# Optimization experiments

Measured on AMD Instinct MI355X. Metric: run time of the kernel, lower is better.

## Reference

```python
import jax, jax.numpy as jnp
import numpy as np

B, N, H, W = 8, 16384, 64, 64
CTX, OUT, ST = 32, 2, 1
HID = [516, 256, 128, 64, 32, 16]
IN_SIZE = CTX + 2 + ST + OUT  # 37


def _bilinear_sample(img, coord):
    """torch F.grid_sample, mode=bilinear, padding=zeros, align_corners=False.
    img: [B,C,H,W]; coord: [B,N,2] (x,y in [-1,1]). Returns [B,C,N]."""
    _, _, Hh, Ww = img.shape
    gx = (coord[..., 0] + 1.0) * (Ww * 0.5) - 0.5
    gy = (coord[..., 1] + 1.0) * (Hh * 0.5) - 0.5
    x0 = jnp.floor(gx)
    y0 = jnp.floor(gy)
    wx1 = gx - x0
    wy1 = gy - y0

    def tap(xi, yi, w):
        valid = (xi >= 0) & (xi < Ww) & (yi >= 0) & (yi < Hh)
        xc = jnp.clip(xi, 0, Ww - 1).astype(jnp.int32)
        yc = jnp.clip(yi, 0, Hh - 1).astype(jnp.int32)
        vals = jax.vmap(lambda im, y, x: im[:, y, x])(img, yc, xc)  # [B,C,N]
        return vals * (w * valid)[:, None, :]

    return (tap(x0, y0, (1 - wx1) * (1 - wy1))
            + tap(x0 + 1, y0, wx1 * (1 - wy1))
            + tap(x0, y0 + 1, (1 - wx1) * wy1)
            + tap(x0 + 1, y0 + 1, wx1 * wy1))


def _layer_shapes():
    shapes = [(IN_SIZE, HID[0])]
    for i in range(len(HID) - 1):
        shapes.append((HID[i] + IN_SIZE, HID[i + 1]))
    shapes.append((HID[-1], OUT))
    return shapes


def setup_inputs():
    key = jax.random.key(0)
    ks = jax.random.split(key, 4 + 7)
    inp = {
        "lr_fields": jax.random.normal(ks[0], (B, OUT, H, W), jnp.float32),
        "context_grid": jax.random.normal(ks[1], (B, CTX, H, W), jnp.float32),
        "hr_eps": jax.random.normal(ks[2], (B, H, W), jnp.float32),
        "coord": jax.random.uniform(ks[3], (B, N, 2), jnp.float32, -1.0, 1.0),
    }
    for j, (fi, fo) in enumerate(_layer_shapes()):
        inp[f"W{j}"] = jax.random.normal(ks[4 + j], (fi, fo), jnp.float32) / np.sqrt(fi)
        inp[f"b{j}"] = jnp.zeros((fo,), jnp.float32)
    return inp


def reference(lr_fields, context_grid, hr_eps, coord,
              W0, b0, W1, b1, W2, b2, W3, b3, W4, b4, W5, b5, W6, b6):
    # original permutes (0,1,3,2) before grid_sample -> swap spatial axes
    ctx_pts = _bilinear_sample(jnp.swapaxes(context_grid, 2, 3), coord)  # [B,CTX,N]
    lr_pts = _bilinear_sample(jnp.swapaxes(lr_fields, 2, 3), coord)      # [B,OUT,N]
    eps_pts = _bilinear_sample(jnp.swapaxes(hr_eps[:, None], 2, 3), coord)  # [B,1,N]
    x_in = jnp.concatenate([
        jnp.transpose(ctx_pts, (0, 2, 1)),
        coord,
        jnp.transpose(lr_pts, (0, 2, 1)),
        jnp.transpose(eps_pts, (0, 2, 1)),
    ], axis=2)  # [B,N,37]
    x = jax.nn.relu(x_in @ W0 + b0)
    for Wl, bl in ((W1, b1), (W2, b2), (W3, b3), (W4, b4), (W5, b5)):
        x = jax.nn.relu(jnp.concatenate([x, x_in], axis=2) @ Wl + bl)
    return x @ W6 + b6  # [B,N,2]
```

## Files before the change

kernel.cpp:

```cpp
#include <hip/hip_runtime.h>


#define NTH     1024
#define NWAVES  16
#define MPTS    64
#define MTILES  (MPTS / 16)
#define SROW    616
#define XIN_OFF 0
#define HSEG    64
#define NPOINTS (8 * 16384)
#define GRIDX   (NPOINTS / MPTS)
#define LDSBYTES (MPTS * SROW * 2)
#define CLSTRIDE 40
#define CLOFF   524288

typedef short          short8  __attribute__((ext_vector_type(8)));
typedef short          short4v __attribute__((ext_vector_type(4)));
typedef float          f32x4   __attribute__((ext_vector_type(4)));
typedef unsigned short u16;

__device__ __forceinline__ u16 f2bf(float f) {
    unsigned int u = __builtin_bit_cast(unsigned int, f);
    u += 0x7fffu + ((u >> 16) & 1u);
    return (u16)(u >> 16);
}

__device__ __forceinline__ unsigned cvtpk(float a, float b) {
    unsigned r;
    asm("v_cvt_pk_bf16_f32 %0, %1, %2" : "=v"(r) : "v"(a), "v"(b));
    return r;
}

__constant__ int pk_base8[8] = {0, 4224, 23680, 28800, 30336, 30848, 31040, 31104};
__constant__ int pk_ks[7]    = {2, 19, 10, 6, 4, 3, 1};
__constant__ int pk_khp[7]   = {0, 544, 256, 128, 64, 32, 32};
__constant__ int pk_kact[7]  = {0, 516, 256, 128, 64, 32, 16};
__constant__ int pk_nact[7]  = {516, 256, 128, 64, 32, 16, 2};

struct WPtrs { const float* W[7]; };

__global__ void pack_weights(WPtrs wp, u16* __restrict__ out)
{
    const int f = blockIdx.x * blockDim.x + threadIdx.x;
    if (f >= 31104) return;
    int l = 0;
    while (l < 6 && f >= pk_base8[l + 1]) ++l;
    const int r    = f - pk_base8[l];
    const int lane = r & 63;
    const int t    = r >> 6;
    const int ks   = pk_ks[l];
    const int s    = t % ks;
    const int nt   = t / ks;
    const int n    = nt * 16 + (lane & 15);
    const int k0   = s * 32 + (lane >> 4) * 8;
    const int nact = pk_nact[l];
    const int khp  = pk_khp[l];
    const int kact = pk_kact[l];
    const float* W = wp.W[l];

    union { short8 v; u16 e[8]; } frag;
#pragma unroll
    for (int j = 0; j < 8; ++j) {
        const int k = k0 + j;
        float v = 0.0f;
        if (n < nact) {
            if (k < khp) {
                if (k < kact) v = W[k * nact + n];
            } else {
                const int xr = k - khp;
                if (xr < 37) v = W[(kact + xr) * nact + n];
            }
        }
        frag.e[j] = f2bf(v);
    }
    *(short8*)(out + (size_t)f * 8) = frag.v;
}

struct RPk { const float* ctx; const float* lr; const float* eps; float* cl; };

__global__ void repack_cl(RPk q)
{
    __shared__ float ls[64 * CLSTRIDE];
    const int b = blockIdx.x >> 6;
    const int x = blockIdx.x & 63;
    for (int i = threadIdx.x; i < 64 * CLSTRIDE; i += 256) ls[i] = 0.f;
    __syncthreads();
    for (int i = threadIdx.x; i < 35 * 64; i += 256) {
        const int c = i / 64, y = i % 64;
        float v; int slot;
        if (c < 32)      { v = q.ctx[(((size_t)b * 32 + c) * 64 + x) * 64 + y]; slot = c; }
        else if (c < 34) { v = q.lr [(((size_t)b * 2 + (c - 32)) * 64 + x) * 64 + y]; slot = 34 + (c - 32); }
        else             { v = q.eps[(((size_t)b) * 64 + x) * 64 + y];          slot = 36; }
        ls[y * CLSTRIDE + slot] = v;
    }
    __syncthreads();
    float* out = q.cl + ((size_t)b * 64 + x) * 64 * CLSTRIDE;
    for (int i = threadIdx.x; i < 64 * CLSTRIDE; i += 256) out[i] = ls[i];
}

struct MainParams {
    const float* lr;
    const float* ctx;
    const float* eps;
    const float* coord;
    const float* Bb[7];
    const u16*   wpack;
    const float* cl;
    int          clok;
    float*       out;
};

template<int NACT, bool RELU>
__device__ __forceinline__ void store_nt(const f32x4* accm,
                                         const float* __restrict__ bias,
                                         u16* __restrict__ s_act,
                                         int nt, int mbase, int lm, int lq)
{
    const int bn = nt * 16 + lq * 4;
    float bv[4];
    if (bn + 4 <= NACT) {
        const f32x4 b4 = *(const f32x4*)(bias + bn);
        bv[0] = b4[0]; bv[1] = b4[1]; bv[2] = b4[2]; bv[3] = b4[3];
    } else {
#pragma unroll
        for (int r = 0; r < 4; ++r)
            bv[r] = (bn + r < NACT) ? bias[bn + r] : 0.f;
    }
#pragma unroll
    for (int m = 0; m < 2; ++m) {
        float v[4];
#pragma unroll
        for (int r = 0; r < 4; ++r) {
            v[r] = accm[m][r] + bv[r];
            if (RELU) v[r] = fmaxf(v[r], 0.f);
        }
        uint2 o;
        o.x = cvtpk(v[0], v[1]);
        o.y = cvtpk(v[2], v[3]);
        *(uint2*)(s_act + (size_t)((mbase + m) * 16 + lm) * SROW + HSEG + bn) = o;
    }
}

template<int KHP, int NT, int NACT, int LBASE,
         bool XIN, bool RELU, bool GOUT, bool IPBAR>
__device__ __forceinline__ void mlayer(const u16* __restrict__ wpack,
                                       const float* __restrict__ bias,
                                       u16* __restrict__ s_act,
                                       float* __restrict__ gout, int p0,
                                       int wave, int lane)
{
    constexpr int KHS = KHP / 32;
    constexpr int KS  = KHS + (XIN ? 2 : 0);
    const int lm = lane & 15;
    const int lq = lane >> 4;
    const int mg = wave & 1;
    const int ng = wave >> 1;
    const int mbase = mg * 2;

    const u16* arow0 = s_act + (size_t)((mbase * 16) + lm) * SROW + lq * 8;
    const u16* arow1 = arow0 + (size_t)16 * SROW;
    const u16* wl = wpack + LBASE + lane * 8;

#define ABOFF(s_) (((s_) < KHS) ? (HSEG + (s_) * 32) : (XIN_OFF + ((s_) - KHS) * 32))

    if constexpr (IPBAR) {
        const int nt0 = ng, nt1 = ng + 8;
        const bool act0 = nt0 < NT;
        const bool act1 = nt1 < NT;
        f32x4 acc[2][2];
#pragma unroll
        for (int i = 0; i < 2; ++i)
#pragma unroll
            for (int m = 0; m < 2; ++m)
                acc[i][m] = (f32x4){0.f, 0.f, 0.f, 0.f};

        if (act0) {
            const u16* bp0 = wl + (size_t)nt0 * KS * 512;
            const u16* bp1 = wl + (size_t)nt1 * KS * 512;
#pragma unroll
            for (int s = 0; s < KS; ++s) {
                const int ab = ABOFF(s);
                const short8 a0 = *(const short8*)(arow0 + ab);
                const short8 a1 = *(const short8*)(arow1 + ab);
                const short8 w0 = *(const short8*)(bp0 + (size_t)s * 512);
                acc[0][0] = __builtin_amdgcn_mfma_f32_16x16x32_bf16(w0, a0, acc[0][0], 0, 0, 0);
                acc[0][1] = __builtin_amdgcn_mfma_f32_16x16x32_bf16(w0, a1, acc[0][1], 0, 0, 0);
                if (act1) {
                    const short8 w1 = *(const short8*)(bp1 + (size_t)s * 512);
                    acc[1][0] = __builtin_amdgcn_mfma_f32_16x16x32_bf16(w1, a0, acc[1][0], 0, 0, 0);
                    acc[1][1] = __builtin_amdgcn_mfma_f32_16x16x32_bf16(w1, a1, acc[1][1], 0, 0, 0);
                }
            }
        }
        __syncthreads();
        if (act0) store_nt<NACT, RELU>(acc[0], bias, s_act, nt0, mbase, lm, lq);
        if (act1) store_nt<NACT, RELU>(acc[1], bias, s_act, nt1, mbase, lm, lq);
    } else {
        for (int g = 0;; ++g) {
            const int nt0 = ng + 16 * g;
            if (nt0 >= NT) break;
            const int nt1 = nt0 + 8;
            const bool act1 = nt1 < NT;
            f32x4 acc[2][2];
#pragma unroll
            for (int i = 0; i < 2; ++i)
#pragma unroll
                for (int m = 0; m < 2; ++m)
                    acc[i][m] = (f32x4){0.f, 0.f, 0.f, 0.f};

            const u16* bp0 = wl + (size_t)nt0 * KS * 512;
            const u16* bp1 = wl + (size_t)nt1 * KS * 512;
#pragma unroll
            for (int s = 0; s < KS; ++s) {
                const int ab = ABOFF(s);
                const short8 a0 = *(const short8*)(arow0 + ab);
                const short8 a1 = *(const short8*)(arow1 + ab);
                const short8 w0 = *(const short8*)(bp0 + (size_t)s * 512);
                acc[0][0] = __builtin_amdgcn_mfma_f32_16x16x32_bf16(w0, a0, acc[0][0], 0, 0, 0);
                acc[0][1] = __builtin_amdgcn_mfma_f32_16x16x32_bf16(w0, a1, acc[0][1], 0, 0, 0);
                if (act1) {
                    const short8 w1 = *(const short8*)(bp1 + (size_t)s * 512);
                    acc[1][0] = __builtin_amdgcn_mfma_f32_16x16x32_bf16(w1, a0, acc[1][0], 0, 0, 0);
                    acc[1][1] = __builtin_amdgcn_mfma_f32_16x16x32_bf16(w1, a1, acc[1][1], 0, 0, 0);
                }
            }

            if (GOUT) {
                if (lq == 0) {
                    const float b0 = bias[0], b1 = bias[1];
#pragma unroll
                    for (int m = 0; m < 2; ++m) {
                        float2 o;
                        o.x = acc[0][m][0] + b0;
                        o.y = acc[0][m][1] + b1;
                        *(float2*)(gout + (size_t)(p0 + (mbase + m) * 16 + lm) * 2) = o;
                    }
                }
            } else {
                store_nt<NACT, RELU>(acc[0], bias, s_act, nt0, mbase, lm, lq);
                if (act1)
                    store_nt<NACT, RELU>(acc[1], bias, s_act, nt1, mbase, lm, lq);
            }
        }
    }
#undef ABOFF
}

__global__ __launch_bounds__(NTH, 8)
void cont_decoder_mfma(MainParams p)
{
    extern __shared__ u16 s_act[];
    __shared__ int   s_x0[MPTS], s_y0[MPTS];
    __shared__ float s_wx[MPTS], s_wy[MPTS];

    const int tid  = threadIdx.x;
    const int wave = tid >> 6;
    const int lane = tid & 63;
    const int p0   = blockIdx.x * MPTS;
    const int b    = p0 >> 14;

    for (int i = tid; i < MPTS * 43; i += NTH) {
        const int pt = i / 43, c = i % 43;
        const int col = (c < 27) ? (37 + c) : (592 + (c - 27));
        s_act[pt * SROW + col] = 0;
    }

    if (tid < MPTS) {
        const int pt = p0 + tid;
        const float cx = p.coord[2 * pt];
        const float cy = p.coord[2 * pt + 1];
        const float gx = (cx + 1.0f) * 32.0f - 0.5f;
        const float gy = (cy + 1.0f) * 32.0f - 0.5f;
        const float fx0 = floorf(gx), fy0 = floorf(gy);
        s_x0[tid] = (int)fx0;
        s_y0[tid] = (int)fy0;
        s_wx[tid] = gx - fx0;
        s_wy[tid] = gy - fy0;
        s_act[tid * SROW + 32] = f2bf(cx);
        s_act[tid * SROW + 33] = f2bf(cy);
    }
    __syncthreads();

    if (p.clok) {
        const float* cl = p.cl + (size_t)b * 64 * 64 * CLSTRIDE;
        for (int idx = tid; idx < MPTS * 10; idx += NTH) {
            const int t = idx / 10;
            const int q = idx % 10;

            const int   x0 = s_x0[t], y0 = s_y0[t];
            const float wx = s_wx[t], wy = s_wy[t];
            const int x1 = x0 + 1, y1 = y0 + 1;
            const bool xv0 = (x0 >= 0) & (x0 < 64);
            const bool xv1 = (x1 >= 0) & (x1 < 64);
            const bool yv0 = (y0 >= 0) & (y0 < 64);
            const bool yv1 = (y1 >= 0) & (y1 < 64);
            const int xc0 = min(max(x0, 0), 63), xc1 = min(max(x1, 0), 63);
            const int yc0 = min(max(y0, 0), 63), yc1 = min(max(y1, 0), 63);

            const float w00 = (1.0f - wx) * (1.0f - wy) * ((xv0 && yv0) ? 1.0f : 0.0f);
            const float w10 = wx * (1.0f - wy)          * ((xv1 && yv0) ? 1.0f : 0.0f);
            const float w01 = (1.0f - wx) * wy          * ((xv0 && yv1) ? 1.0f : 0.0f);
            const float w11 = wx * wy                   * ((xv1 && yv1) ? 1.0f : 0.0f);

            const int qo = q * 4;
            const f32x4 t00 = *(const f32x4*)(cl + (size_t)(xc0 * 64 + yc0) * CLSTRIDE + qo);
            const f32x4 t10 = *(const f32x4*)(cl + (size_t)(xc1 * 64 + yc0) * CLSTRIDE + qo);
            const f32x4 t01 = *(const f32x4*)(cl + (size_t)(xc0 * 64 + yc1) * CLSTRIDE + qo);
            const f32x4 t11 = *(const f32x4*)(cl + (size_t)(xc1 * 64 + yc1) * CLSTRIDE + qo);

            const f32x4 v = w00 * t00 + w10 * t10 + w01 * t01 + w11 * t11;
            const unsigned lo = cvtpk(v[0], v[1]);
            const unsigned hi = cvtpk(v[2], v[3]);

            if (q == 8) {
                *(unsigned*)(s_act + (size_t)t * SROW + 34) = hi;
            } else {
                uint2 o; o.x = lo; o.y = hi;
                *(uint2*)(s_act + (size_t)t * SROW + qo) = o;
            }
        }
    } else {
        for (int idx = tid; idx < MPTS * 35; idx += NTH) {
            const int t = idx / 35;
            const int c = idx % 35;
            const float* base;
            int col;
            if (c < 32)      { base = p.ctx + (size_t)(b * 32 + c) * 4096;       col = c; }
            else if (c < 34) { base = p.lr  + (size_t)(b * 2 + (c - 32)) * 4096; col = 34 + (c - 32); }
            else             { base = p.eps + (size_t)b * 4096;                   col = 36; }

            const int   x0 = s_x0[t], y0 = s_y0[t];
            const float wx = s_wx[t], wy = s_wy[t];
            const int x1 = x0 + 1, y1 = y0 + 1;
            const bool xv0 = (x0 >= 0) & (x0 < 64);
            const bool xv1 = (x1 >= 0) & (x1 < 64);
            const bool yv0 = (y0 >= 0) & (y0 < 64);
            const bool yv1 = (y1 >= 0) & (y1 < 64);
            const int xc0 = min(max(x0, 0), 63), xc1 = min(max(x1, 0), 63);
            const int yc0 = min(max(y0, 0), 63), yc1 = min(max(y1, 0), 63);

            const float w00 = (1.0f - wx) * (1.0f - wy) * ((xv0 && yv0) ? 1.0f : 0.0f);
            const float w10 = wx * (1.0f - wy)          * ((xv1 && yv0) ? 1.0f : 0.0f);
            const float w01 = (1.0f - wx) * wy          * ((xv0 && yv1) ? 1.0f : 0.0f);
            const float w11 = wx * wy                   * ((xv1 && yv1) ? 1.0f : 0.0f);

            const float val = w00 * base[xc0 * 64 + yc0]
                            + w10 * base[xc1 * 64 + yc0]
                            + w01 * base[xc0 * 64 + yc1]
                            + w11 * base[xc1 * 64 + yc1];
            s_act[t * SROW + col] = f2bf(val);
        }
    }
    __syncthreads();

    mlayer<  0, 33, 516, 0,      true,  true,  false, false>(p.wpack, p.Bb[0], s_act, nullptr, p0, wave, lane);
    __syncthreads();
    mlayer<544, 16, 256, 33792,  true,  true,  false, true >(p.wpack, p.Bb[1], s_act, nullptr, p0, wave, lane);
    __syncthreads();
    mlayer<256,  8, 128, 189440, true,  true,  false, true >(p.wpack, p.Bb[2], s_act, nullptr, p0, wave, lane);
    __syncthreads();
    mlayer<128,  4,  64, 230400, true,  true,  false, true >(p.wpack, p.Bb[3], s_act, nullptr, p0, wave, lane);
    __syncthreads();
    mlayer< 64,  2,  32, 242688, true,  true,  false, true >(p.wpack, p.Bb[4], s_act, nullptr, p0, wave, lane);
    __syncthreads();
    mlayer< 32,  1,  16, 246784, true,  true,  false, true >(p.wpack, p.Bb[5], s_act, nullptr, p0, wave, lane);
    __syncthreads();
    mlayer< 32,  1,   2, 248320, false, false, true,  false>(p.wpack, p.Bb[6], s_act, p.out,   p0, wave, lane);
}

extern "C" void kernel_launch(void* const* d_in, const int* in_sizes, int n_in,
                              void* d_out, int out_size, void* d_ws, size_t ws_size,
                              hipStream_t stream)
{
    WPtrs wp;
    for (int l = 0; l < 7; ++l) wp.W[l] = (const float*)d_in[4 + 2 * l];

    const size_t cl_bytes = (size_t)8 * 64 * 64 * CLSTRIDE * 4;
    const bool clok = ws_size >= (size_t)CLOFF + cl_bytes;

    MainParams p;
    p.lr    = (const float*)d_in[0];
    p.ctx   = (const float*)d_in[1];
    p.eps   = (const float*)d_in[2];
    p.coord = (const float*)d_in[3];
    for (int l = 0; l < 7; ++l) p.Bb[l] = (const float*)d_in[5 + 2 * l];
    p.wpack = (const u16*)d_ws;
    p.cl    = (const float*)((const char*)d_ws + CLOFF);
    p.clok  = clok ? 1 : 0;
    p.out   = (float*)d_out;

    hipFuncSetAttribute((const void*)cont_decoder_mfma,
                        hipFuncAttributeMaxDynamicSharedMemorySize, LDSBYTES);

    hipLaunchKernelGGL(pack_weights, dim3(122), dim3(256), 0, stream, wp, (u16*)d_ws);
    if (clok) {
        RPk q;
        q.ctx = p.ctx; q.lr = p.lr; q.eps = p.eps;
        q.cl  = (float*)((char*)d_ws + CLOFF);
        hipLaunchKernelGGL(repack_cl, dim3(512), dim3(256), 0, stream, q);
    }
    hipLaunchKernelGGL(cont_decoder_mfma, dim3(GRIDX), dim3(NTH), LDSBYTES, stream, p);
}
```

Measured before the change: 184.4 us.

## Merge prep kernels, ping-pong activation buffers to drop intra-layer barriers, widen gather loads

Fuses the weight-pack and context-repack kernels into one launch to save a kernel launch. In the MLP, layers 2-5 now read their hidden input from one LDS region and write output to a different offset (ping-pong), so they no longer need the barrier between the MFMA loop and the store. The bilinear gather now has each thread handle 8 channels instead of 4 and write 16-byte LDS stores. The risks are overlapping LDS regions if the chosen offsets are wrong, and a bit more register pressure in the gather.

```diff
diff --git a/kernel.cpp b/kernel.cpp
--- a/kernel.cpp
+++ b/kernel.cpp
@@ -7,7 +7,6 @@
 #define MTILES  (MPTS / 16)
 #define SROW    616
 #define XIN_OFF 0
-#define HSEG    64
 #define NPOINTS (8 * 16384)
 #define GRIDX   (NPOINTS / MPTS)
 #define LDSBYTES (MPTS * SROW * 2)
@@ -15,8 +14,8 @@
 #define CLOFF   524288
 
 typedef short          short8  __attribute__((ext_vector_type(8)));
-typedef short          short4v __attribute__((ext_vector_type(4)));
 typedef float          f32x4   __attribute__((ext_vector_type(4)));
+typedef unsigned int   u32x4   __attribute__((ext_vector_type(4)));
 typedef unsigned short u16;
 
 __device__ __forceinline__ u16 f2bf(float f) {
@@ -38,64 +37,65 @@
 __constant__ int pk_nact[7]  = {516, 256, 128, 64, 32, 16, 2};
 
 struct WPtrs { const float* W[7]; };
-
-__global__ void pack_weights(WPtrs wp, u16* __restrict__ out)
-{
-    const int f = blockIdx.x * blockDim.x + threadIdx.x;
-    if (f >= 31104) return;
-    int l = 0;
-    while (l < 6 && f >= pk_base8[l + 1]) ++l;
-    const int r    = f - pk_base8[l];
-    const int lane = r & 63;
-    const int t    = r >> 6;
-    const int ks   = pk_ks[l];
-    const int s    = t % ks;
-    const int nt   = t / ks;
-    const int n    = nt * 16 + (lane & 15);
-    const int k0   = s * 32 + (lane >> 4) * 8;
-    const int nact = pk_nact[l];
-    const int khp  = pk_khp[l];
-    const int kact = pk_kact[l];
-    const float* W = wp.W[l];
-
-    union { short8 v; u16 e[8]; } frag;
-#pragma unroll
-    for (int j = 0; j < 8; ++j) {
-        const int k = k0 + j;
-        float v = 0.0f;
-        if (n < nact) {
-            if (k < khp) {
-                if (k < kact) v = W[k * nact + n];
-            } else {
-                const int xr = k - khp;
-                if (xr < 37) v = W[(kact + xr) * nact + n];
-            }
-        }
-        frag.e[j] = f2bf(v);
-    }
-    *(short8*)(out + (size_t)f * 8) = frag.v;
-}
-
 struct RPk { const float* ctx; const float* lr; const float* eps; float* cl; };
 
-__global__ void repack_cl(RPk q)
+__global__ void prep_ws(WPtrs wp, RPk q, u16* __restrict__ out, int clok)
 {
     __shared__ float ls[64 * CLSTRIDE];
-    const int b = blockIdx.x >> 6;
-    const int x = blockIdx.x & 63;
-    for (int i = threadIdx.x; i < 64 * CLSTRIDE; i += 256) ls[i] = 0.f;
-    __syncthreads();
-    for (int i = threadIdx.x; i < 35 * 64; i += 256) {
-        const int c = i / 64, y = i % 64;
-        float v; int slot;
-        if (c < 32)      { v = q.ctx[(((size_t)b * 32 + c) * 64 + x) * 64 + y]; slot = c; }
-        else if (c < 34) { v = q.lr [(((size_t)b * 2 + (c - 32)) * 64 + x) * 64 + y]; slot = 34 + (c - 32); }
-        else             { v = q.eps[(((size_t)b) * 64 + x) * 64 + y];          slot = 36; }
-        ls[y * CLSTRIDE + slot] = v;
-    }
-    __syncthreads();
-    float* out = q.cl + ((size_t)b * 64 + x) * 64 * CLSTRIDE;
-    for (int i = threadIdx.x; i < 64 * CLSTRIDE; i += 256) out[i] = ls[i];
+
+    if (blockIdx.x < 122) {
+        const int f = blockIdx.x * blockDim.x + threadIdx.x;
+        if (f >= 31104) return;
+        int l = 0;
+        while (l < 6 && f >= pk_base8[l + 1]) ++l;
+        const int r    = f - pk_base8[l];
+        const int lane = r & 63;
+        const int t    = r >> 6;
+        const int ks   = pk_ks[l];
+        const int s    = t % ks;
+        const int nt   = t / ks;
+        const int n    = nt * 16 + (lane & 15);
+        const int k0   = s * 32 + (lane >> 4) * 8;
+        const int nact = pk_nact[l];
+        const int khp  = pk_khp[l];
+        const int kact = pk_kact[l];
+        const float* W = wp.W[l];
+
+        union { short8 v; u16 e[8]; } frag;
+#pragma unroll
+        for (int j = 0; j < 8; ++j) {
+            const int k = k0 + j;
+            float v = 0.0f;
+            if (n < nact) {
+                if (k < khp) {
+                    if (k < kact) v = W[k * nact + n];
+                } else {
+                    const int xr = k - khp;
+                    if (xr < 37) v = W[(kact + xr) * nact + n];
+                }
+            }
+            frag.e[j] = f2bf(v);
+        }
+        *(short8*)(out + (size_t)f * 8) = frag.v;
+    } else {
+        if (!clok) return;
+        const int bx = blockIdx.x - 122;
+        const int b = bx >> 6;
+        const int x = bx & 63;
+        for (int i = threadIdx.x; i < 64 * CLSTRIDE; i += 256) ls[i] = 0.f;
+        __syncthreads();
+        for (int i = threadIdx.x; i < 35 * 64; i += 256) {
+            const int c = i / 64, y = i % 64;
+            float v; int slot;
+            if (c < 32)      { v = q.ctx[(((size_t)b * 32 + c) * 64 + x) * 64 + y]; slot = c; }
+            else if (c < 34) { v = q.lr [(((size_t)b * 2 + (c - 32)) * 64 + x) * 64 + y]; slot = 34 + (c - 32); }
+            else             { v = q.eps[(((size_t)b) * 64 + x) * 64 + y];          slot = 36; }
+            ls[y * CLSTRIDE + slot] = v;
+        }
+        __syncthreads();
+        float* o = q.cl + ((size_t)b * 64 + x) * 64 * CLSTRIDE;
+        for (int i = threadIdx.x; i < 64 * CLSTRIDE; i += 256) o[i] = ls[i];
+    }
 }
 
 struct MainParams {
@@ -110,7 +110,7 @@
     float*       out;
 };
 
-template<int NACT, bool RELU>
+template<int OS, int NACT, bool RELU>
 __device__ __forceinline__ void store_nt(const f32x4* accm,
                                          const float* __restrict__ bias,
                                          u16* __restrict__ s_act,
@@ -137,11 +137,11 @@
         uint2 o;
         o.x = cvtpk(v[0], v[1]);
         o.y = cvtpk(v[2], v[3]);
-        *(uint2*)(s_act + (size_t)((mbase + m) * 16 + lm) * SROW + HSEG + bn) = o;
-    }
-}
-
-template<int KHP, int NT, int NACT, int LBASE,
+        *(uint2*)(s_act + (size_t)((mbase + m) * 16 + lm) * SROW + OS + bn) = o;
+    }
+}
+
+template<int KHP, int HS, int OS, int NT, int NACT, int LBASE,
          bool XIN, bool RELU, bool GOUT, bool IPBAR>
 __device__ __forceinline__ void mlayer(const u16* __restrict__ wpack,
                                        const float* __restrict__ bias,
@@ -161,20 +161,21 @@
     const u16* arow1 = arow0 + (size_t)16 * SROW;
     const u16* wl = wpack + LBASE + lane * 8;
 
-#define ABOFF(s_) (((s_) < KHS) ? (HSEG + (s_) * 32) : (XIN_OFF + ((s_) - KHS) * 32))
-
-    if constexpr (IPBAR) {
-        const int nt0 = ng, nt1 = ng + 8;
-        const bool act0 = nt0 < NT;
-        const bool act1 = nt1 < NT;
-        f32x4 acc[2][2];
-#pragma unroll
-        for (int i = 0; i < 2; ++i)
-#pragma unroll
-            for (int m = 0; m < 2; ++m)
-                acc[i][m] = (f32x4){0.f, 0.f, 0.f, 0.f};
-
-        if (act0) {
+#define ABOFF(s_) (((s_) < KHS) ? (HS + (s_) * 32) : (XIN_OFF + ((s_) - KHS) * 32))
+
+    if constexpr (NT > 16) {
+        for (int g = 0;; ++g) {
+            const int nt0 = ng + 16 * g;
+            if (nt0 >= NT) break;
+            const int nt1 = nt0 + 8;
+            const bool act1 = nt1 < NT;
+            f32x4 acc[2][2];
+#pragma unroll
+            for (int i = 0; i < 2; ++i)
+#pragma unroll
+                for (int m = 0; m < 2; ++m)
+                    acc[i][m] = (f32x4){0.f, 0.f, 0.f, 0.f};
+
             const u16* bp0 = wl + (size_t)nt0 * KS * 512;
             const u16* bp1 = wl + (size_t)nt1 * KS * 512;
 #pragma unroll
@@ -191,23 +192,22 @@
                     acc[1][1] = __builtin_amdgcn_mfma_f32_16x16x32_bf16(w1, a1, acc[1][1], 0, 0, 0);
                 }
             }
-        }
-        __syncthreads();
-        if (act0) store_nt<NACT, RELU>(acc[0], bias, s_act, nt0, mbase, lm, lq);
-        if (act1) store_nt<NACT, RELU>(acc[1], bias, s_act, nt1, mbase, lm, lq);
+            store_nt<OS, NACT, RELU>(acc[0], bias, s_act, nt0, mbase, lm, lq);
+            if (act1)
+                store_nt<OS, NACT, RELU>(acc[1], bias, s_act, nt1, mbase, lm, lq);
+        }
     } else {
-        for (int g = 0;; ++g) {
-            const int nt0 = ng + 16 * g;
-            if (nt0 >= NT) break;
-            const int nt1 = nt0 + 8;
-            const bool act1 = nt1 < NT;
-            f32x4 acc[2][2];
-#pragma unroll
-            for (int i = 0; i < 2; ++i)
-#pragma unroll
-                for (int m = 0; m < 2; ++m)
-                    acc[i][m] = (f32x4){0.f, 0.f, 0.f, 0.f};
-
+        const int nt0 = ng, nt1 = ng + 8;
+        const bool act0 = nt0 < NT;
+        const bool act1 = nt1 < NT;
+        f32x4 acc[2][2];
+#pragma unroll
+        for (int i = 0; i < 2; ++i)
+#pragma unroll
+            for (int m = 0; m < 2; ++m)
+                acc[i][m] = (f32x4){0.f, 0.f, 0.f, 0.f};
+
+        if (act0) {
             const u16* bp0 = wl + (size_t)nt0 * KS * 512;
             const u16* bp1 = wl + (size_t)nt1 * KS * 512;
 #pragma unroll
@@ -224,23 +224,22 @@
                     acc[1][1] = __builtin_amdgcn_mfma_f32_16x16x32_bf16(w1, a1, acc[1][1], 0, 0, 0);
                 }
             }
-
-            if (GOUT) {
-                if (lq == 0) {
-                    const float b0 = bias[0], b1 = bias[1];
-#pragma unroll
-                    for (int m = 0; m < 2; ++m) {
-                        float2 o;
-                        o.x = acc[0][m][0] + b0;
-                        o.y = acc[0][m][1] + b1;
-                        *(float2*)(gout + (size_t)(p0 + (mbase + m) * 16 + lm) * 2) = o;
-                    }
+        }
+        if constexpr (IPBAR) __syncthreads();
+        if (GOUT) {
+            if (act0 && lq == 0) {
+                const float b0 = bias[0], b1 = bias[1];
+#pragma unroll
+                for (int m = 0; m < 2; ++m) {
+                    float2 o;
+                    o.x = acc[0][m][0] + b0;
+                    o.y = acc[0][m][1] + b1;
+                    *(float2*)(gout + (size_t)(p0 + (mbase + m) * 16 + lm) * 2) = o;
                 }
-            } else {
-                store_nt<NACT, RELU>(acc[0], bias, s_act, nt0, mbase, lm, lq);
-                if (act1)
-                    store_nt<NACT, RELU>(acc[1], bias, s_act, nt1, mbase, lm, lq);
             }
+        } else {
+            if (act0) store_nt<OS, NACT, RELU>(acc[0], bias, s_act, nt0, mbase, lm, lq);
+            if (act1) store_nt<OS, NACT, RELU>(acc[1], bias, s_act, nt1, mbase, lm, lq);
         }
     }
 #undef ABOFF
@@ -283,9 +282,9 @@
 
     if (p.clok) {
         const float* cl = p.cl + (size_t)b * 64 * 64 * CLSTRIDE;
-        for (int idx = tid; idx < MPTS * 10; idx += NTH) {
-            const int t = idx / 10;
-            const int q = idx % 10;
+        for (int idx = tid; idx < MPTS * 5; idx += NTH) {
+            const int t  = idx / 5;
+            const int it = idx % 5;
 
             const int   x0 = s_x0[t], y0 = s_y0[t];
             const float wx = s_wx[t], wy = s_wy[t];
@@ -302,21 +301,34 @@
             const float w01 = (1.0f - wx) * wy          * ((xv0 && yv1) ? 1.0f : 0.0f);
             const float w11 = wx * wy                   * ((xv1 && yv1) ? 1.0f : 0.0f);
 
-            const int qo = q * 4;
-            const f32x4 t00 = *(const f32x4*)(cl + (size_t)(xc0 * 64 + yc0) * CLSTRIDE + qo);
-            const f32x4 t10 = *(const f32x4*)(cl + (size_t)(xc1 * 64 + yc0) * CLSTRIDE + qo);
-            const f32x4 t01 = *(const f32x4*)(cl + (size_t)(xc0 * 64 + yc1) * CLSTRIDE + qo);
-            const f32x4 t11 = *(const f32x4*)(cl + (size_t)(xc1 * 64 + yc1) * CLSTRIDE + qo);
-
-            const f32x4 v = w00 * t00 + w10 * t10 + w01 * t01 + w11 * t11;
-            const unsigned lo = cvtpk(v[0], v[1]);
-            const unsigned hi = cvtpk(v[2], v[3]);
-
-            if (q == 8) {
-                *(unsigned*)(s_act + (size_t)t * SROW + 34) = hi;
+            const float* c00 = cl + (size_t)(xc0 * 64 + yc0) * CLSTRIDE;
+            const float* c10 = cl + (size_t)(xc1 * 64 + yc0) * CLSTRIDE;
+            const float* c01 = cl + (size_t)(xc0 * 64 + yc1) * CLSTRIDE;
+            const float* c11 = cl + (size_t)(xc1 * 64 + yc1) * CLSTRIDE;
+
+            const int qo = it * 8;
+            const f32x4 v0 = w00 * *(const f32x4*)(c00 + qo)
+                           + w10 * *(const f32x4*)(c10 + qo)
+                           + w01 * *(const f32x4*)(c01 + qo)
+                           + w11 * *(const f32x4*)(c11 + qo);
+            const f32x4 v1 = w00 * *(const f32x4*)(c00 + qo + 4)
+                           + w10 * *(const f32x4*)(c10 + qo + 4)
+                           + w01 * *(const f32x4*)(c01 + qo + 4)
+                           + w11 * *(const f32x4*)(c11 + qo + 4);
+
+            if (it == 4) {
+                *(unsigned*)(s_act + (size_t)t * SROW + 34) = cvtpk(v0[2], v0[3]);
+                uint2 o;
+                o.x = cvtpk(v1[0], v1[1]);
+                o.y = cvtpk(v1[2], v1[3]);
+                *(uint2*)(s_act + (size_t)t * SROW + 36) = o;
             } else {
-                uint2 o; o.x = lo; o.y = hi;
-                *(uint2*)(s_act + (size_t)t * SROW + qo) = o;
+                u32x4 o;
+                o.x = cvtpk(v0[0], v0[1]);
+                o.y = cvtpk(v0[2], v0[3]);
+                o.z = cvtpk(v1[0], v1[1]);
+                o.w = cvtpk(v1[2], v1[3]);
+                *(u32x4*)(s_act + (size_t)t * SROW + qo) = o;
             }
         }
     } else {
@@ -353,19 +365,19 @@
     }
     __syncthreads();
 
-    mlayer<  0, 33, 516, 0,      true,  true,  false, false>(p.wpack, p.Bb[0], s_act, nullptr, p0, wave, lane);
-    __syncthreads();
-    mlayer<544, 16, 256, 33792,  true,  true,  false, true >(p.wpack, p.Bb[1], s_act, nullptr, p0, wave, lane);
-    __syncthreads();
-    mlayer<256,  8, 128, 189440, true,  true,  false, true >(p.wpack, p.Bb[2], s_act, nullptr, p0, wave, lane);
-    __syncthreads();
-    mlayer<128,  4,  64, 230400, true,  true,  false, true >(p.wpack, p.Bb[3], s_act, nullptr, p0, wave, lane);
-    __syncthreads();
-    mlayer< 64,  2,  32, 242688, true,  true,  false, true >(p.wpack, p.Bb[4], s_act, nullptr, p0, wave, lane);
-    __syncthreads();
-    mlayer< 32,  1,  16, 246784, true,  true,  false, true >(p.wpack, p.Bb[5], s_act, nullptr, p0, wave, lane);
-    __syncthreads();
-    mlayer< 32,  1,   2, 248320, false, false, true,  false>(p.wpack, p.Bb[6], s_act, p.out,   p0, wave, lane);
+    mlayer<  0,  64,  64, 33, 516, 0,      true,  true,  false, false>(p.wpack, p.Bb[0], s_act, nullptr, p0, wave, lane);
+    __syncthreads();
+    mlayer<544,  64,  64, 16, 256, 33792,  true,  true,  false, true >(p.wpack, p.Bb[1], s_act, nullptr, p0, wave, lane);
+    __syncthreads();
+    mlayer<256,  64, 320,  8, 128, 189440, true,  true,  false, false>(p.wpack, p.Bb[2], s_act, nullptr, p0, wave, lane);
+    __syncthreads();
+    mlayer<128, 320,  64,  4,  64, 230400, true,  true,  false, false>(p.wpack, p.Bb[3], s_act, nullptr, p0, wave, lane);
+    __syncthreads();
+    mlayer< 64,  64, 448,  2,  32, 242688, true,  true,  false, false>(p.wpack, p.Bb[4], s_act, nullptr, p0, wave, lane);
+    __syncthreads();
+    mlayer< 32, 448, 128,  1,  16, 246784, true,  true,  false, false>(p.wpack, p.Bb[5], s_act, nullptr, p0, wave, lane);
+    __syncthreads();
+    mlayer< 32, 128,   0,  1,   2, 248320, false, false, true,  false>(p.wpack, p.Bb[6], s_act, p.out,   p0, wave, lane);
 }
 
 extern "C" void kernel_launch(void* const* d_in, const int* in_sizes, int n_in,
@@ -389,15 +401,14 @@
     p.clok  = clok ? 1 : 0;
     p.out   = (float*)d_out;
 
+    RPk q;
+    q.ctx = p.ctx; q.lr = p.lr; q.eps = p.eps;
+    q.cl  = (float*)((char*)d_ws + CLOFF);
+
     hipFuncSetAttribute((const void*)cont_decoder_mfma,
                         hipFuncAttributeMaxDynamicSharedMemorySize, LDSBYTES);
 
-    hipLaunchKernelGGL(pack_weights, dim3(122), dim3(256), 0, stream, wp, (u16*)d_ws);
-    if (clok) {
-        RPk q;
-        q.ctx = p.ctx; q.lr = p.lr; q.eps = p.eps;
-        q.cl  = (float*)((char*)d_ws + CLOFF);
-        hipLaunchKernelGGL(repack_cl, dim3(512), dim3(256), 0, stream, q);
-    }
+    hipLaunchKernelGGL(prep_ws, dim3(122 + 512), dim3(256), 0, stream,
+                       wp, q, (u16*)d_ws, clok ? 1 : 0);
     hipLaunchKernelGGL(cont_decoder_mfma, dim3(GRIDX), dim3(NTH), LDSBYTES, stream, p);
 }
```

After: 180.0 us. 2.4% less time.
